# Performance work log

Measured on AMD Instinct MI355X. Metric: run time of the kernel, lower is better.

Reference implementation:

```python
import jax, jax.numpy as jnp
import numpy as np

N_NODES = 10000
N_EDGES = 160000
N_GRAPHS = 64
F = 80        # hidden dim
T = 5         # towers
F_OUT = 16    # per-tower post output (80/5)
N_LAYERS = 4
EPS = 1e-6
BN_EPS = 1e-5
STD_EPS = 1e-5


def setup_inputs() -> dict:
    key = jax.random.key(0)
    ks = jax.random.split(key, 12)
    x = jax.random.uniform(ks[0], (N_NODES, 2), dtype=jnp.float32)
    edge_index = jax.random.randint(ks[1], (2, N_EDGES), 0, N_NODES, dtype=jnp.int64)
    batch = jnp.sort(jax.random.randint(ks[2], (N_NODES,), 0, N_GRAPHS, dtype=jnp.int64))

    def w(k, shape, fan_in):
        return (jax.random.normal(k, shape, jnp.float32) / np.float32(np.sqrt(fan_in)))

    return {
        "x": x, "edge_index": edge_index, "batch": batch,
        "pre_lin_W": w(ks[3], (1, F), 1), "pre_lin_b": jnp.zeros((F,), jnp.float32),
        "pre_W": w(ks[4], (N_LAYERS, T, 2 * F, F), 2 * F), "pre_b": jnp.zeros((N_LAYERS, T, F), jnp.float32),
        "post_W": w(ks[5], (N_LAYERS, T, 13 * F, F_OUT), 13 * F), "post_b": jnp.zeros((N_LAYERS, T, F_OUT), jnp.float32),
        "lin_W": w(ks[6], (N_LAYERS, F, F), F), "lin_b": jnp.zeros((N_LAYERS, F), jnp.float32),
        "bn_gamma": jnp.ones((N_LAYERS, F), jnp.float32), "bn_beta": jnp.zeros((N_LAYERS, F), jnp.float32),
        "mlp_lin_W": w(ks[7], (40, 1), 40), "mlp_lin_b": jnp.zeros((1,), jnp.float32),
        "mlp1_W": w(ks[8], (40, 20), 40), "mlp1_b": jnp.zeros((20,), jnp.float32),
        "mlp2_W": w(ks[9], (20, 1), 20), "mlp2_b": jnp.zeros((1,), jnp.float32),
    }


def _pna_conv(h, src, dst, deg, avg_log_deg, preW, preb, postW, postb, linW, linb):
    # h: [N, F]; messages per tower: pre MLP over cat(x_i, x_j)  (divide_input=False)
    N = h.shape[0]
    hm = jnp.concatenate([h[dst], h[src]], axis=-1)            # [E, 2F]
    m = jnp.einsum('ef,tfo->eto', hm, preW) + preb             # [E, T, F]

    cnt = jnp.maximum(deg, 1.0)[:, None, None]                 # [N,1,1]
    has = (deg > 0)[:, None, None]
    s = jax.ops.segment_sum(m, dst, num_segments=N)
    mean = s / cnt
    mean_sq = jax.ops.segment_sum(m * m, dst, num_segments=N) / cnt
    mn = jax.ops.segment_min(m, dst, num_segments=N)
    mx = jax.ops.segment_max(m, dst, num_segments=N)
    mn = jnp.where(has, mn, 0.0)
    mx = jnp.where(has, mx, 0.0)
    std = jnp.sqrt(jax.nn.relu(mean_sq - mean * mean) + STD_EPS)
    agg = jnp.concatenate([mean, mn, mx, std], axis=-1)        # [N, T, 4F]

    logd = jnp.log(jnp.maximum(deg, 1.0) + 1.0)[:, None, None]
    amp = agg * (logd / avg_log_deg)
    att = agg * (avg_log_deg / logd)
    out = jnp.concatenate([agg, amp, att], axis=-1)            # [N, T, 12F]

    xt = jnp.broadcast_to(h[:, None, :], (N, T, F))
    out = jnp.concatenate([xt, out], axis=-1)                  # [N, T, 13F]
    out = jnp.einsum('ntf,tfo->nto', out, postW) + postb       # [N, T, F_OUT]
    out = out.reshape(N, T * F_OUT)                            # [N, 80]
    return out @ linW + linb


def _forward(x, edge_index, batch, pre_lin_W, pre_lin_b, pre_W, pre_b,
             post_W, post_b, lin_W, lin_b, bn_gamma, bn_beta,
             mlp_lin_W, mlp_lin_b, mlp1_W, mlp1_b, mlp2_W, mlp2_b):
    N = x.shape[0]
    src, dst = edge_index[0], edge_index[1]
    deg = jax.ops.segment_sum(jnp.ones_like(dst, jnp.float32), dst, num_segments=N)
    avg_log_deg = jnp.mean(jnp.log(deg + 1.0))                 # PNA avg log-degree from deg histogram

    operation = x[:, 0:1]
    assignment = x[:, 1:2]
    op = operation @ pre_lin_W + pre_lin_b                     # [N, 80]

    for l in range(N_LAYERS):
        y = _pna_conv(op, src, dst, deg, avg_log_deg,
                      pre_W[l], pre_b[l], post_W[l], post_b[l], lin_W[l], lin_b[l])
        mu = jnp.mean(y, axis=0)
        var = jnp.mean((y - mu) ** 2, axis=0)                  # biased, training-mode BN
        y = (y - mu) / jnp.sqrt(var + BN_EPS) * bn_gamma[l] + bn_beta[l]
        op = jax.nn.relu(y)

    front, behind = op[:, :40], op[:, 40:]
    xc = front * assignment + behind                           # [N, 40], non-negative

    # LastLayer: log-space scatter-add message passing
    log_score = jax.ops.segment_sum(jnp.log(xc[src] + EPS), dst, num_segments=N)
    xc = jnp.exp(log_score + jnp.log(xc + EPS))

    # global mean pool over graphs
    gcnt = jnp.maximum(jax.ops.segment_sum(jnp.ones_like(batch, jnp.float32), batch, num_segments=N_GRAPHS), 1.0)
    pooled = jax.ops.segment_sum(xc, batch, num_segments=N_GRAPHS) / gcnt[:, None]  # [B, 40]

    x_lin = pooled @ mlp_lin_W + mlp_lin_b
    x_cv = pooled @ mlp1_W + mlp1_b
    x_cv = 20.0 - jax.nn.relu(x_cv)
    x_cv = x_cv @ mlp2_W + mlp2_b
    return x_cv + x_lin                                        # [B, 1]


def reference(x, edge_index, batch, pre_lin_W, pre_lin_b, pre_W, pre_b,
              post_W, post_b, lin_W, lin_b, bn_gamma, bn_beta,
              mlp_lin_W, mlp_lin_b, mlp1_W, mlp1_b, mlp2_W, mlp2_b):
    return _forward(x, edge_index, batch, pre_lin_W, pre_lin_b, pre_W, pre_b,
                    post_W, post_b, lin_W, lin_b, bn_gamma, bn_beta,
                    mlp_lin_W, mlp_lin_b, mlp1_W, mlp1_b, mlp2_W, mlp2_b)
```

## Files before the change

### kernel.cpp

```cpp
#include <hip/hip_runtime.h>
#include <math.h>

#define NN 10000
#define NE 160000
#define NG 64
#define FEAT 80
#define NT 5
#define NL 4

__global__ void k_cnt2(const int* __restrict__ dst, const int* __restrict__ batch,
                       int* __restrict__ deg, int* __restrict__ gcnt) {
    int e = blockIdx.x * 256 + threadIdx.x;
    if (e < NE) atomicAdd(&deg[dst[e]], 1);
    if (e < NN) atomicAdd(&gcnt[batch[e]], 1);
}

__global__ void k_scan(const int* __restrict__ deg, int* __restrict__ offs) {
    __shared__ int sums[256];
    int tid = threadIdx.x;
    int start = tid * 40, stop = min(start + 40, NN);
    int s = 0;
    for (int i = start; i < stop; ++i) s += deg[i];
    sums[tid] = s;
    __syncthreads();
    for (int off = 1; off < 256; off <<= 1) {
        int v = (tid >= off) ? sums[tid - off] : 0;
        __syncthreads();
        sums[tid] += v;
        __syncthreads();
    }
    int base = (tid == 0) ? 0 : sums[tid - 1];
    for (int i = start; i < stop; ++i) { offs[i] = base; base += deg[i]; }
    if (tid == 255) offs[NN] = sums[255];
}

__global__ void k_ald(const int* __restrict__ deg, float* __restrict__ ald) {
    __shared__ float red[256];
    int i = blockIdx.x * 256 + threadIdx.x;
    red[threadIdx.x] = (i < NN) ? logf((float)deg[i] + 1.0f) : 0.0f;
    __syncthreads();
    for (int s = 128; s > 0; s >>= 1) {
        if (threadIdx.x < s) red[threadIdx.x] += red[threadIdx.x + s];
        __syncthreads();
    }
    if (threadIdx.x == 0) atomicAdd(ald, red[0]);
}

__global__ void k_fill(const int* __restrict__ src, const int* __restrict__ dst,
                       const int* __restrict__ offs, int* __restrict__ cursor,
                       int* __restrict__ csr) {
    int e = blockIdx.x * 256 + threadIdx.x;
    if (e < NE) {
        int d = dst[e];
        int p = atomicAdd(&cursor[d], 1);
        csr[offs[d] + p] = src[e];
    }
}

__global__ void k_op0(const float* __restrict__ x, const float* __restrict__ plW,
                      const float* __restrict__ plb, float* __restrict__ hT) {
    int i = blockIdx.x * 256 + threadIdx.x;
    if (i < FEAT * NN) {
        int f = i / NN, n = i - f * NN;
        hT[i] = x[2 * n] * plW[f] + plb[f];
    }
}

__global__ __launch_bounds__(256) void k_mm_ab(
        const float* __restrict__ hT, const float* __restrict__ preW_l,
        float* __restrict__ A, float* __restrict__ Bt) {
    __shared__ float hs[16][80];
    int n0 = blockIdx.x * 16;
    int tid = threadIdx.x;
    for (int i = tid; i < 16 * 80; i += 256) {
        int nl = i & 15, f = i >> 4;
        hs[nl][f] = hT[(size_t)f * NN + n0 + nl];
    }
    __syncthreads();
    int c0 = blockIdx.y * 512 + tid;
    float acc[2][16];
#pragma unroll
    for (int s = 0; s < 2; s++)
#pragma unroll
        for (int i = 0; i < 16; i++) acc[s][i] = 0.f;
    const float* wp[2];
#pragma unroll
    for (int s = 0; s < 2; s++) {
        int c = c0 + s * 256;
        int part = (c >= 400) ? 1 : 0;
        int cc = c - part * 400;
        int t = cc / 80, o = cc - t * 80;
        wp[s] = preW_l + (size_t)(t * 160 + part * 80) * 80 + o;
    }
    bool act1 = (c0 + 256) < 800;
    for (int fq = 0; fq < 80; fq += 4) {
        float w0a = wp[0][(fq + 0) * 80], w0b = wp[0][(fq + 1) * 80];
        float w0c = wp[0][(fq + 2) * 80], w0d = wp[0][(fq + 3) * 80];
        float w1a = 0.f, w1b = 0.f, w1c = 0.f, w1d = 0.f;
        if (act1) {
            w1a = wp[1][(fq + 0) * 80]; w1b = wp[1][(fq + 1) * 80];
            w1c = wp[1][(fq + 2) * 80]; w1d = wp[1][(fq + 3) * 80];
        }
#pragma unroll
        for (int i = 0; i < 16; i++) {
            float4 hv = *(const float4*)&hs[i][fq];
            acc[0][i] += hv.x * w0a + hv.y * w0b + hv.z * w0c + hv.w * w0d;
            acc[1][i] += hv.x * w1a + hv.y * w1b + hv.z * w1c + hv.w * w1d;
        }
    }
#pragma unroll
    for (int s = 0; s < 2; s++) {
        int c = c0 + s * 256;
        if (c < 800) {
            int part = (c >= 400) ? 1 : 0;
            int cc = c - part * 400;
            int t = cc / 80, o = cc - t * 80;
            if (part == 0) {
#pragma unroll
                for (int i = 0; i < 16; i++) A[(size_t)(n0 + i) * 400 + cc] = acc[s][i];
            } else {
#pragma unroll
                for (int i = 0; i < 16; i++)
                    Bt[((size_t)t * NN + n0 + i) * 80 + o] = acc[s][i];
            }
        }
    }
}

__global__ __launch_bounds__(256) void k_agg_t(
        const float* __restrict__ A, const float* __restrict__ Bt,
        const int* __restrict__ offs, const int* __restrict__ csr,
        const float* __restrict__ preb_l, float* __restrict__ aggT) {
    __shared__ float st[320 * 17];
    int tid = threadIdx.x;
    int t = blockIdx.y;
    int n0 = blockIdx.x * 16;
    int ni = tid >> 4;
    int cl = tid & 15;
    int n = n0 + ni;
    int e0 = offs[n], e1 = offs[n + 1];
    const float* Bts = Bt + (size_t)t * NN * 80;
    float s[5], q[5], mn[5], mx[5];
#pragma unroll
    for (int k = 0; k < 5; k++) { s[k] = 0.f; q[k] = 0.f; mn[k] = 3.4e38f; mx[k] = -3.4e38f; }
    int e = e0;
    for (; e + 3 < e1; e += 4) {
        const float* br0 = Bts + (size_t)csr[e] * 80 + cl;
        const float* br1 = Bts + (size_t)csr[e + 1] * 80 + cl;
        const float* br2 = Bts + (size_t)csr[e + 2] * 80 + cl;
        const float* br3 = Bts + (size_t)csr[e + 3] * 80 + cl;
#pragma unroll
        for (int k = 0; k < 5; k++) {
            float b0 = br0[k * 16];
            float b1 = br1[k * 16];
            float b2 = br2[k * 16];
            float b3 = br3[k * 16];
            s[k] += (b0 + b1) + (b2 + b3);
            q[k] += (b0 * b0 + b1 * b1) + (b2 * b2 + b3 * b3);
            mn[k] = fminf(mn[k], fminf(fminf(b0, b1), fminf(b2, b3)));
            mx[k] = fmaxf(mx[k], fmaxf(fmaxf(b0, b1), fmaxf(b2, b3)));
        }
    }
    for (; e < e1; ++e) {
        const float* br = Bts + (size_t)csr[e] * 80 + cl;
#pragma unroll
        for (int k = 0; k < 5; k++) {
            float b = br[k * 16];
            s[k] += b; q[k] += b * b;
            mn[k] = fminf(mn[k], b); mx[k] = fmaxf(mx[k], b);
        }
    }
    int d = e1 - e0;
    float degf = (float)d;
    float cnt = fmaxf(degf, 1.f);
#pragma unroll
    for (int k = 0; k < 5; k++) {
        int c = cl + k * 16;
        float a = A[(size_t)n * 400 + t * 80 + c] + preb_l[t * 80 + c];
        float mean = (degf * a + s[k]) / cnt;
        float msq  = (degf * a * a + 2.f * a * s[k] + q[k]) / cnt;
        float sd = sqrtf(fmaxf(msq - mean * mean, 0.f) + 1e-5f);
        float mnr = (d > 0) ? a + mn[k] : 0.f;
        float mxr = (d > 0) ? a + mx[k] : 0.f;
        st[(0 * 80 + c) * 17 + ni] = mean;
        st[(1 * 80 + c) * 17 + ni] = mnr;
        st[(2 * 80 + c) * 17 + ni] = mxr;
        st[(3 * 80 + c) * 17 + ni] = sd;
    }
    __syncthreads();
    int jj = tid >> 4;
    int nl = tid & 15;
#pragma unroll
    for (int pass = 0; pass < 20; ++pass) {
        int j = pass * 16 + jj;
        aggT[((size_t)t * 320 + j) * NN + n0 + nl] = st[j * 17 + nl];
    }
}

__global__ __launch_bounds__(256) void k_post(
        const float* __restrict__ hT, const float* __restrict__ aggT,
        const float* __restrict__ postW_l, const float* __restrict__ postb_l,
        const int* __restrict__ offs, const float* __restrict__ ald_sum,
        float* __restrict__ y0T) {
    __shared__ float wj[80 * 48];
    __shared__ float wh[80 * 16];
    int tid = threadIdx.x;
    int t = blockIdx.y;
    int jq = blockIdx.z;
    int j0 = jq * 80;
    const float* W0 = postW_l + (size_t)t * 1040 * 16;
    const float* W1 = W0 + 80 * 16;
    const float* W2 = W0 + 400 * 16;
    const float* W3 = W0 + 720 * 16;
    for (int idx = tid; idx < 80 * 48; idx += 256) {
        int j = idx / 48;
        int rem = idx - j * 48;
        int p = rem >> 4, o = rem & 15;
        const float* Wp = (p == 0) ? W1 : (p == 1) ? W2 : W3;
        wj[idx] = Wp[(j0 + j) * 16 + o];
    }
    if (jq == 0) {
        for (int idx = tid; idx < 80 * 16; idx += 256)
            wh[idx] = W0[idx];
    }
    __syncthreads();
    int n = blockIdx.x * 256 + tid;
    bool alive = (n < NN);
    int nc = alive ? n : 0;
    float acc1[16], acc2[16], acc3[16];
#pragma unroll
    for (int i = 0; i < 16; i++) { acc1[i] = 0.f; acc2[i] = 0.f; acc3[i] = 0.f; }
    const float* ap = aggT + ((size_t)t * 320 + j0) * NN + nc;
#pragma unroll 8
    for (int j = 0; j < 80; ++j) {
        float a = ap[(size_t)j * NN];
        const float* w = wj + j * 48;
#pragma unroll
        for (int i = 0; i < 16; i++) {
            acc1[i] += a * w[i];
            acc2[i] += a * w[16 + i];
            acc3[i] += a * w[32 + i];
        }
    }
    if (jq == 0) {
#pragma unroll 4
        for (int f = 0; f < 80; ++f) {
            float hv = hT[(size_t)f * NN + nc];
            const float* w = wh + f * 16;
#pragma unroll
            for (int i = 0; i < 16; i++) acc1[i] += hv * w[i];
        }
    }
    if (alive) {
        float degf = (float)(offs[n + 1] - offs[n]);
        float ald = ald_sum[0] * (1.f / NN);
        float logd = logf(fmaxf(degf, 1.f) + 1.f);
        float c1 = logd / ald;
        float c2 = ald / logd;
#pragma unroll
        for (int i = 0; i < 16; i++) {
            float v = acc1[i] + c1 * acc2[i] + c2 * acc3[i];
            if (jq == 0) v += postb_l[t * 16 + i];
            unsafeAtomicAdd(&y0T[(size_t)(t * 16 + i) * NN + n], v);
        }
    }
}

__global__ __launch_bounds__(256) void k_lin(
        const float* __restrict__ y0T, const float* __restrict__ linW_l,
        const float* __restrict__ linb_l, float* __restrict__ yT) {
    __shared__ float ws[80 * 8];
    int tid = threadIdx.x;
    int f0 = blockIdx.y * 8;
    for (int idx = tid; idx < 80 * 8; idx += 256)
        ws[idx] = linW_l[(idx >> 3) * 80 + f0 + (idx & 7)];
    __syncthreads();
    int n = blockIdx.x * 256 + tid;
    bool alive = (n < NN);
    int nc = alive ? n : 0;
    float acc[8];
#pragma unroll
    for (int i = 0; i < 8; i++) acc[i] = 0.f;
#pragma unroll 8
    for (int k = 0; k < 80; ++k) {
        float v = y0T[(size_t)k * NN + nc];
        const float4 wa = *(const float4*)(ws + k * 8);
        const float4 wb = *(const float4*)(ws + k * 8 + 4);
        acc[0] += v * wa.x; acc[1] += v * wa.y; acc[2] += v * wa.z; acc[3] += v * wa.w;
        acc[4] += v * wb.x; acc[5] += v * wb.y; acc[6] += v * wb.z; acc[7] += v * wb.w;
    }
    if (alive) {
#pragma unroll
        for (int i = 0; i < 8; i++)
            yT[(size_t)(f0 + i) * NN + n] = acc[i] + linb_l[f0 + i];
    }
}

__global__ void k_bnstats(const float* __restrict__ yT, float* __restrict__ bnst) {
    __shared__ float r1[256], r2[256];
    int f = blockIdx.x;
    int seg = blockIdx.y;
    int tid = threadIdx.x;
    int i0 = seg * 1250, i1 = min(i0 + 1250, NN);
    float s = 0.f, q = 0.f;
    for (int i = i0 + tid; i < i1; i += 256) {
        float v = yT[(size_t)f * NN + i];
        s += v; q += v * v;
    }
    r1[tid] = s; r2[tid] = q;
    __syncthreads();
    for (int st = 128; st > 0; st >>= 1) {
        if (tid < st) { r1[tid] += r1[tid + st]; r2[tid] += r2[tid + st]; }
        __syncthreads();
    }
    if (tid == 0) {
        unsafeAtomicAdd(&bnst[f], r1[0]);
        unsafeAtomicAdd(&bnst[80 + f], r2[0]);
    }
}

__global__ void k_bn(const float* __restrict__ yT, const float* __restrict__ bnst,
                     const float* __restrict__ gamma_l, const float* __restrict__ beta_l,
                     float* __restrict__ hT) {
    int i = blockIdx.x * 256 + threadIdx.x;
    if (i >= FEAT * NN) return;
    int f = i / NN;
    float mu = bnst[f] * (1.f / NN);
    float msq = bnst[80 + f] * (1.f / NN);
    float var = fmaxf(msq - mu * mu, 0.f);
    float v = (yT[i] - mu) * (1.f / sqrtf(var + 1e-5f)) * gamma_l[f] + beta_l[f];
    hT[i] = fmaxf(v, 0.f);
}

__global__ void k_bnxc(const float* __restrict__ yT, const float* __restrict__ bnst,
                       const float* __restrict__ gamma_l, const float* __restrict__ beta_l,
                       const float* __restrict__ x, float* __restrict__ lxc) {
    int i = blockIdx.x * 256 + threadIdx.x;
    if (i >= 40 * NN) return;
    int f = i / NN, n = i - f * NN;
    int f2 = f + 40;
    float mu1 = bnst[f] * (1.f / NN);
    float ms1 = bnst[80 + f] * (1.f / NN);
    float v1 = (yT[(size_t)f * NN + n] - mu1) *
               (1.f / sqrtf(fmaxf(ms1 - mu1 * mu1, 0.f) + 1e-5f)) * gamma_l[f] + beta_l[f];
    v1 = fmaxf(v1, 0.f);
    float mu2 = bnst[f2] * (1.f / NN);
    float ms2 = bnst[80 + f2] * (1.f / NN);
    float v2 = (yT[(size_t)f2 * NN + n] - mu2) *
               (1.f / sqrtf(fmaxf(ms2 - mu2 * mu2, 0.f) + 1e-5f)) * gamma_l[f2] + beta_l[f2];
    v2 = fmaxf(v2, 0.f);
    lxc[(size_t)n * 40 + f] = logf(v1 * x[2 * n + 1] + v2 + 1e-6f);
}

__global__ void k_logagg(const float* __restrict__ lxc, const int* __restrict__ offs,
                         const int* __restrict__ csr, const int* __restrict__ batch,
                         float* __restrict__ pooled) {
    int n = blockIdx.x;
    int tid = threadIdx.x;
    if (tid >= 40) return;
    int e0 = offs[n], e1 = offs[n + 1];
    float s = 0.f;
    for (int k = e0; k < e1; ++k) s += lxc[(size_t)csr[k] * 40 + tid];
    float v = expf(s + lxc[(size_t)n * 40 + tid]);
    atomicAdd(&pooled[batch[n] * 40 + tid], v);
}

__global__ void k_final(const float* __restrict__ pooled, const int* __restrict__ gcnt,
                        const float* __restrict__ mlW, const float* __restrict__ mlb,
                        const float* __restrict__ m1W, const float* __restrict__ m1b,
                        const float* __restrict__ m2W, const float* __restrict__ m2b,
                        float* __restrict__ out) {
    int g = threadIdx.x;
    if (g >= NG) return;
    float inv = 1.f / fmaxf((float)gcnt[g], 1.f);
    float pl[40];
#pragma unroll
    for (int j = 0; j < 40; j++) pl[j] = pooled[g * 40 + j] * inv;
    float xl = mlb[0];
#pragma unroll
    for (int j = 0; j < 40; j++) xl += pl[j] * mlW[j];
    float acc = m2b[0];
    for (int k = 0; k < 20; k++) {
        float v = m1b[k];
#pragma unroll
        for (int j = 0; j < 40; j++) v += pl[j] * m1W[j * 20 + k];
        v = 20.f - fmaxf(v, 0.f);
        acc += v * m2W[k];
    }
    out[g] = acc + xl;
}

extern "C" void kernel_launch(void* const* d_in, const int* in_sizes, int n_in,
                              void* d_out, int out_size, void* d_ws, size_t ws_size,
                              hipStream_t stream) {
    const float* x     = (const float*)d_in[0];
    const int*   ei    = (const int*)d_in[1];
    const int*   batch = (const int*)d_in[2];
    const float* plW   = (const float*)d_in[3];
    const float* plb   = (const float*)d_in[4];
    const float* preW  = (const float*)d_in[5];
    const float* preb  = (const float*)d_in[6];
    const float* postW = (const float*)d_in[7];
    const float* postb = (const float*)d_in[8];
    const float* linW  = (const float*)d_in[9];
    const float* linb  = (const float*)d_in[10];
    const float* bnG   = (const float*)d_in[11];
    const float* bnB   = (const float*)d_in[12];
    const float* mlW   = (const float*)d_in[13];
    const float* mlb   = (const float*)d_in[14];
    const float* m1W   = (const float*)d_in[15];
    const float* m1b   = (const float*)d_in[16];
    const float* m2W   = (const float*)d_in[17];
    const float* m2b   = (const float*)d_in[18];
    float* out = (float*)d_out;
    const int* srcp = ei;
    const int* dstp = ei + NE;

    char* p = (char*)d_ws;
    int*   deg    = (int*)(p + 0);
    int*   cursor = (int*)(p + 40000);
    int*   gcnt   = (int*)(p + 80000);
    float* ald    = (float*)(p + 80256);
    float* pooled = (float*)(p + 80272);
    float* bnst   = (float*)(p + 90512);
    int*   offs   = (int*)(p + 93072);
    int*   csr    = (int*)(p + 133088);
    float* hT     = (float*)(p + 773088);
    float* A      = (float*)(p + 3973088);
    float* Bt     = (float*)(p + 19973088);
    float* aggT   = (float*)(p + 35973088);
    float* y0T = (float*)(p + 23173088);
    float* yT  = (float*)(p + 26373088);
    float* lxc = (float*)(p + 35973088);

    hipMemsetAsync(d_ws, 0, 93072, stream);
    k_cnt2<<<dim3((NE + 255) / 256), 256, 0, stream>>>(dstp, batch, deg, gcnt);
    k_scan<<<1, 256, 0, stream>>>(deg, offs);
    k_ald<<<dim3((NN + 255) / 256), 256, 0, stream>>>(deg, ald);
    k_fill<<<dim3((NE + 255) / 256), 256, 0, stream>>>(srcp, dstp, offs, cursor, csr);
    k_op0<<<dim3((FEAT * NN + 255) / 256), 256, 0, stream>>>(x, plW, plb, hT);

    for (int l = 0; l < NL; ++l) {
        const float* preW_l  = preW  + (size_t)l * NT * 160 * 80;
        const float* preb_l  = preb  + l * NT * 80;
        const float* postW_l = postW + (size_t)l * NT * 1040 * 16;
        const float* postb_l = postb + l * NT * 16;
        const float* linW_l  = linW  + l * 80 * 80;
        const float* linb_l  = linb  + l * 80;
        float* bnst_l = bnst + l * 160;
        k_mm_ab<<<dim3(625, 2), 256, 0, stream>>>(hT, preW_l, A, Bt);
        k_agg_t<<<dim3(625, 5), 256, 0, stream>>>(A, Bt, offs, csr, preb_l, aggT);
        hipMemsetAsync(y0T, 0, (size_t)80 * NN * 4, stream);
        k_post<<<dim3(40, 5, 4), 256, 0, stream>>>(hT, aggT, postW_l, postb_l, offs, ald, y0T);
        k_lin<<<dim3(40, 10), 256, 0, stream>>>(y0T, linW_l, linb_l, yT);
        k_bnstats<<<dim3(80, 8), 256, 0, stream>>>(yT, bnst_l);
        if (l < NL - 1) {
            k_bn<<<dim3((FEAT * NN + 255) / 256), 256, 0, stream>>>(
                yT, bnst_l, bnG + l * 80, bnB + l * 80, hT);
        } else {
            k_bnxc<<<dim3((40 * NN + 255) / 256), 256, 0, stream>>>(
                yT, bnst_l, bnG + l * 80, bnB + l * 80, x, lxc);
        }
    }

    k_logagg<<<dim3(NN), 64, 0, stream>>>(lxc, offs, csr, batch, pooled);
    k_final<<<1, 64, 0, stream>>>(pooled, gcnt, mlW, mlb, m1W, m1b, m2W, m2b, out);
}
```

Baseline: 835.2 us.

## Fold post-tower h weights into lin via precomputed matrix and tile k_post

Precomputes Wh = postW_h · linW per layer, so the h contribution is added in k_lin directly instead of being accumulated inside k_post with per-tower weights. k_post now stages aggT tiles and weight chunks in shared memory with float4 loads, and each thread computes a 4-node × 4-output register tile rather than one node × 16 outputs. The goal is to cut redundant global loads and the per-tower hT reads, and to balance work across the jq blocks. The cost is an extra small kernel launch per layer, an extra 80-deep loop in k_lin, and more block synchronizations in k_post.

```diff
diff --git a/kernel.cpp b/kernel.cpp
--- a/kernel.cpp
+++ b/kernel.cpp
@@ -197,83 +197,130 @@
     }
 }
 
+__global__ void k_wh(const float* __restrict__ postW_l, const float* __restrict__ linW_l,
+                     float* __restrict__ Wh) {
+    int f = blockIdx.x;
+    int fo = threadIdx.x;
+    if (fo >= 80) return;
+    float s = 0.f;
+    for (int t = 0; t < NT; ++t) {
+        const float* w0 = postW_l + ((size_t)t * 1040 + f) * 16;
+#pragma unroll
+        for (int o2 = 0; o2 < 16; ++o2)
+            s += w0[o2] * linW_l[(t * 16 + o2) * 80 + fo];
+    }
+    Wh[f * 80 + fo] = s;
+}
+
 __global__ __launch_bounds__(256) void k_post(
-        const float* __restrict__ hT, const float* __restrict__ aggT,
-        const float* __restrict__ postW_l, const float* __restrict__ postb_l,
-        const int* __restrict__ offs, const float* __restrict__ ald_sum,
-        float* __restrict__ y0T) {
-    __shared__ float wj[80 * 48];
-    __shared__ float wh[80 * 16];
-    int tid = threadIdx.x;
+        const float* __restrict__ aggT, const float* __restrict__ postW_l,
+        const float* __restrict__ postb_l, const int* __restrict__ offs,
+        const float* __restrict__ ald_sum, float* __restrict__ y0T) {
+    __shared__ float stile[16 * 256];
+    __shared__ float wjs[16 * 48];
+    __shared__ float c1s[256], c2s[256];
+    int tid = threadIdx.x;
+    int nl = tid & 63;
+    int oq = tid >> 6;
     int t = blockIdx.y;
     int jq = blockIdx.z;
+    int n0 = blockIdx.x * 256;
     int j0 = jq * 80;
-    const float* W0 = postW_l + (size_t)t * 1040 * 16;
-    const float* W1 = W0 + 80 * 16;
-    const float* W2 = W0 + 400 * 16;
-    const float* W3 = W0 + 720 * 16;
-    for (int idx = tid; idx < 80 * 48; idx += 256) {
-        int j = idx / 48;
-        int rem = idx - j * 48;
-        int p = rem >> 4, o = rem & 15;
-        const float* Wp = (p == 0) ? W1 : (p == 1) ? W2 : W3;
-        wj[idx] = Wp[(j0 + j) * 16 + o];
-    }
-    if (jq == 0) {
-        for (int idx = tid; idx < 80 * 16; idx += 256)
-            wh[idx] = W0[idx];
-    }
-    __syncthreads();
-    int n = blockIdx.x * 256 + tid;
-    bool alive = (n < NN);
-    int nc = alive ? n : 0;
+    const float* W1 = postW_l + (size_t)t * 1040 * 16 + 80 * 16;
+    const float* W2 = W1 + 320 * 16;
+    const float* W3 = W2 + 320 * 16;
+    {
+        int n = n0 + tid;
+        float ald = ald_sum[0] * (1.f / NN);
+        if (n < NN) {
+            float degf = (float)(offs[n + 1] - offs[n]);
+            float logd = logf(fmaxf(degf, 1.f) + 1.f);
+            c1s[tid] = logd / ald;
+            c2s[tid] = ald / logd;
+        } else { c1s[tid] = 0.f; c2s[tid] = 0.f; }
+    }
     float acc1[16], acc2[16], acc3[16];
 #pragma unroll
     for (int i = 0; i < 16; i++) { acc1[i] = 0.f; acc2[i] = 0.f; acc3[i] = 0.f; }
-    const float* ap = aggT + ((size_t)t * 320 + j0) * NN + nc;
-#pragma unroll 8
-    for (int j = 0; j < 80; ++j) {
-        float a = ap[(size_t)j * NN];
-        const float* w = wj + j * 48;
-#pragma unroll
-        for (int i = 0; i < 16; i++) {
-            acc1[i] += a * w[i];
-            acc2[i] += a * w[16 + i];
-            acc3[i] += a * w[32 + i];
-        }
-    }
-    if (jq == 0) {
+    bool full = (n0 + 256 <= NN);
+    for (int jc = 0; jc < 80; jc += 16) {
+        __syncthreads();
+#pragma unroll
+        for (int k = 0; k < 4; ++k) {
+            int idx = k * 256 + tid;
+            int j = idx >> 6;
+            int n4 = (idx & 63) * 4;
+            const float* rowp = aggT + ((size_t)(t * 320 + j0 + jc + j)) * NN + n0;
+            float4 v;
+            if (full) {
+                v = *(const float4*)(rowp + n4);
+            } else {
+                v.x = (n0 + n4     < NN) ? rowp[n4]     : 0.f;
+                v.y = (n0 + n4 + 1 < NN) ? rowp[n4 + 1] : 0.f;
+                v.z = (n0 + n4 + 2 < NN) ? rowp[n4 + 2] : 0.f;
+                v.w = (n0 + n4 + 3 < NN) ? rowp[n4 + 3] : 0.f;
+            }
+            *(float4*)(stile + j * 256 + n4) = v;
+        }
+#pragma unroll
+        for (int k = 0; k < 3; ++k) {
+            int idx = k * 256 + tid;
+            int j = idx / 48;
+            int rem = idx - j * 48;
+            int pp = rem >> 4, o = rem & 15;
+            const float* Wp = (pp == 0) ? W1 : (pp == 1) ? W2 : W3;
+            wjs[idx] = Wp[(j0 + jc + j) * 16 + o];
+        }
+        __syncthreads();
 #pragma unroll 4
-        for (int f = 0; f < 80; ++f) {
-            float hv = hT[(size_t)f * NN + nc];
-            const float* w = wh + f * 16;
-#pragma unroll
-            for (int i = 0; i < 16; i++) acc1[i] += hv * w[i];
-        }
-    }
-    if (alive) {
-        float degf = (float)(offs[n + 1] - offs[n]);
-        float ald = ald_sum[0] * (1.f / NN);
-        float logd = logf(fmaxf(degf, 1.f) + 1.f);
-        float c1 = logd / ald;
-        float c2 = ald / logd;
-#pragma unroll
-        for (int i = 0; i < 16; i++) {
-            float v = acc1[i] + c1 * acc2[i] + c2 * acc3[i];
-            if (jq == 0) v += postb_l[t * 16 + i];
-            unsafeAtomicAdd(&y0T[(size_t)(t * 16 + i) * NN + n], v);
+        for (int j = 0; j < 16; ++j) {
+            float4 sv = *(const float4*)(stile + j * 256 + nl * 4);
+            const float* w = wjs + j * 48 + oq * 4;
+            float4 w1 = *(const float4*)(w);
+            float4 w2 = *(const float4*)(w + 16);
+            float4 w3 = *(const float4*)(w + 32);
+            float sa[4] = {sv.x, sv.y, sv.z, sv.w};
+            float wa1[4] = {w1.x, w1.y, w1.z, w1.w};
+            float wa2[4] = {w2.x, w2.y, w2.z, w2.w};
+            float wa3[4] = {w3.x, w3.y, w3.z, w3.w};
+#pragma unroll
+            for (int ni = 0; ni < 4; ++ni)
+#pragma unroll
+                for (int oi = 0; oi < 4; ++oi) {
+                    acc1[ni * 4 + oi] += sa[ni] * wa1[oi];
+                    acc2[ni * 4 + oi] += sa[ni] * wa2[oi];
+                    acc3[ni * 4 + oi] += sa[ni] * wa3[oi];
+                }
+        }
+    }
+#pragma unroll
+    for (int ni = 0; ni < 4; ++ni) {
+        int nn = n0 + nl * 4 + ni;
+        if (nn < NN) {
+            float c1 = c1s[nl * 4 + ni], c2 = c2s[nl * 4 + ni];
+#pragma unroll
+            for (int oi = 0; oi < 4; ++oi) {
+                int o = oq * 4 + oi;
+                float v = acc1[ni * 4 + oi] + c1 * acc2[ni * 4 + oi] + c2 * acc3[ni * 4 + oi];
+                if (jq == 0) v += postb_l[t * 16 + o];
+                unsafeAtomicAdd(&y0T[(size_t)(t * 16 + o) * NN + nn], v);
+            }
         }
     }
 }
 
 __global__ __launch_bounds__(256) void k_lin(
-        const float* __restrict__ y0T, const float* __restrict__ linW_l,
+        const float* __restrict__ y0T, const float* __restrict__ hT,
+        const float* __restrict__ linW_l, const float* __restrict__ Wh,
         const float* __restrict__ linb_l, float* __restrict__ yT) {
     __shared__ float ws[80 * 8];
+    __shared__ float whs[80 * 8];
     int tid = threadIdx.x;
     int f0 = blockIdx.y * 8;
-    for (int idx = tid; idx < 80 * 8; idx += 256)
-        ws[idx] = linW_l[(idx >> 3) * 80 + f0 + (idx & 7)];
+    for (int idx = tid; idx < 80 * 8; idx += 256) {
+        ws[idx]  = linW_l[(idx >> 3) * 80 + f0 + (idx & 7)];
+        whs[idx] = Wh[(idx >> 3) * 80 + f0 + (idx & 7)];
+    }
     __syncthreads();
     int n = blockIdx.x * 256 + tid;
     bool alive = (n < NN);
@@ -286,6 +333,14 @@
         float v = y0T[(size_t)k * NN + nc];
         const float4 wa = *(const float4*)(ws + k * 8);
         const float4 wb = *(const float4*)(ws + k * 8 + 4);
+        acc[0] += v * wa.x; acc[1] += v * wa.y; acc[2] += v * wa.z; acc[3] += v * wa.w;
+        acc[4] += v * wb.x; acc[5] += v * wb.y; acc[6] += v * wb.z; acc[7] += v * wb.w;
+    }
+#pragma unroll 8
+    for (int k = 0; k < 80; ++k) {
+        float v = hT[(size_t)k * NN + nc];
+        const float4 wa = *(const float4*)(whs + k * 8);
+        const float4 wb = *(const float4*)(whs + k * 8 + 4);
         acc[0] += v * wa.x; acc[1] += v * wa.y; acc[2] += v * wa.z; acc[3] += v * wa.w;
         acc[4] += v * wb.x; acc[5] += v * wb.y; acc[6] += v * wb.z; acc[7] += v * wb.w;
     }
@@ -431,6 +486,7 @@
     float* aggT   = (float*)(p + 35973088);
     float* y0T = (float*)(p + 23173088);
     float* yT  = (float*)(p + 26373088);
+    float* Wh  = (float*)(p + 29573088);
     float* lxc = (float*)(p + 35973088);
 
     hipMemsetAsync(d_ws, 0, 93072, stream);
@@ -451,8 +507,9 @@
         k_mm_ab<<<dim3(625, 2), 256, 0, stream>>>(hT, preW_l, A, Bt);
         k_agg_t<<<dim3(625, 5), 256, 0, stream>>>(A, Bt, offs, csr, preb_l, aggT);
         hipMemsetAsync(y0T, 0, (size_t)80 * NN * 4, stream);
-        k_post<<<dim3(40, 5, 4), 256, 0, stream>>>(hT, aggT, postW_l, postb_l, offs, ald, y0T);
-        k_lin<<<dim3(40, 10), 256, 0, stream>>>(y0T, linW_l, linb_l, yT);
+        k_wh<<<dim3(80), 128, 0, stream>>>(postW_l, linW_l, Wh);
+        k_post<<<dim3(40, 5, 4), 256, 0, stream>>>(aggT, postW_l, postb_l, offs, ald, y0T);
+        k_lin<<<dim3(40, 10), 256, 0, stream>>>(y0T, hT, linW_l, Wh, linb_l, yT);
         k_bnstats<<<dim3(80, 8), 256, 0, stream>>>(yT, bnst_l);
         if (l < NL - 1) {
             k_bn<<<dim3((FEAT * NN + 255) / 256), 256, 0, stream>>>(
```

Result: slower. 930.5 us (+11.4%).
